# Kernel optimization log

Hardware: AMD Instinct MI355X
Metric: run time of the kernel (lower is better)

## Reference

```python
import jax, jax.numpy as jnp
import numpy as np

D_IN = 256
D_OUT = 256

def setup_inputs() -> dict:
    key = jax.random.key(0)
    kx, kq, kk, kv = jax.random.split(key, 4)
    x = jax.random.normal(kx, (8, D_IN, 64, 64), dtype=jnp.float32)
    s = 1.0 / np.sqrt(D_IN)
    Wq = jax.random.normal(kq, (D_OUT, D_IN), dtype=jnp.float32) * s
    Wk = jax.random.normal(kk, (D_OUT, D_IN), dtype=jnp.float32) * s
    Wv = jax.random.normal(kv, (D_OUT, D_IN), dtype=jnp.float32) * s
    return {"x": x, "Wq": Wq, "Wk": Wk, "Wv": Wv}

def reference(x, Wq, Wk, Wv):
    b, c_in, h, w = x.shape
    c = Wq.shape[0]
    # 1x1 conv == channel linear; tokens along N = h*w
    xt = x.reshape(b, c_in, h * w).transpose(0, 2, 1)      # (b, N, c_in)
    q = jnp.einsum('bnc,dc->bnd', xt, Wq)                  # (b, N, c)
    k = jnp.einsum('bnc,dc->bnd', xt, Wk)
    v = jnp.einsum('bnc,dc->bnd', xt, Wv)
    wei = jnp.einsum('bnd,bmd->bnm', q, k) / jnp.sqrt(jnp.asarray(c, x.dtype))
    wei = jax.nn.softmax(wei, axis=-1)
    out = jnp.einsum('bnm,bmd->bnd', wei, v)               # (b, N, c)
    return out.transpose(0, 2, 1).reshape(b, c, h, w)
```

## Files before the change

kernel.cpp:

```cpp
#include <hip/hip_runtime.h>

#define DIN 256
#define NTOK 4096

typedef __bf16 bf16;
typedef __bf16 bf16x8 __attribute__((ext_vector_type(8)));
typedef float floatx16 __attribute__((ext_vector_type(16)));

__device__ inline floatx16 mfma32(bf16x8 a, bf16x8 b, floatx16 c) {
    return __builtin_amdgcn_mfma_f32_32x32x16_bf16(a, b, c, 0, 0, 0);
}

__device__ inline void async16(const void* g, void* l) {
    __builtin_amdgcn_global_load_lds(
        (const __attribute__((address_space(1))) unsigned int*)g,
        (__attribute__((address_space(3))) unsigned int*)l, 16, 0, 0);
}

__global__ void convert_w(const float* __restrict__ wq, const float* __restrict__ wk,
                          const float* __restrict__ wv, bf16* __restrict__ Wb) {
    int i = blockIdx.x * 256 + threadIdx.x;
    const float* src = (i < 65536) ? wq : (i < 131072 ? wk : wv);
    Wb[i] = (bf16)src[i & 65535];
}

__global__ __launch_bounds__(256, 2) void proj_kernel(
    const float* __restrict__ x, const bf16* __restrict__ Wb,
    bf16* __restrict__ Qo, bf16* __restrict__ Ko, bf16* __restrict__ Vo)
{
    __shared__ bf16 xs[64][264];
    __shared__ bf16 wsm[64][264];

    int bid = blockIdx.x;
    int b = bid & 7, nt = bid >> 3;
    int n0 = nt * 64;
    int t = threadIdx.x;
    int lane = t & 63, w = t >> 6;
    int l32 = lane & 31, h = lane >> 5;
    int tokg = w >> 1;
    int og   = w & 1;

    {
        const float* xb = x + (size_t)b * DIN * NTOK;
#pragma unroll
        for (int it = 0; it < 16; ++it) {
            int flat = it * 256 + t;
            int c = flat >> 4;
            int nf = flat & 15;
            float4 v = *(const float4*)(xb + (size_t)c * NTOK + n0 + nf * 4);
            int nn = nf * 4;
            xs[nn + 0][c] = (bf16)v.x;
            xs[nn + 1][c] = (bf16)v.y;
            xs[nn + 2][c] = (bf16)v.z;
            xs[nn + 3][c] = (bf16)v.w;
        }
    }
    __syncthreads();

    bf16x8 xf[16];
#pragma unroll
    for (int ks = 0; ks < 16; ++ks)
        xf[ks] = *(const bf16x8*)&xs[tokg * 32 + l32][ks * 16 + h * 8];

    for (int mat = 0; mat < 3; ++mat) {
        const bf16* Wm = Wb + mat * 65536;
        for (int dg = 0; dg < 4; ++dg) {
            __syncthreads();
#pragma unroll
            for (int it = 0; it < 8; ++it) {
                int flat = it * 256 + t;
                int r = flat >> 5;
                int cs = (flat & 31) * 8;
                *(bf16x8*)&wsm[r][cs] =
                    *(const bf16x8*)(Wm + (size_t)(dg * 64 + r) * 256 + cs);
            }
            __syncthreads();

            floatx16 acc;
#pragma unroll
            for (int i = 0; i < 16; ++i) acc[i] = 0.0f;

            if (mat < 2) {
#pragma unroll
                for (int ks = 0; ks < 16; ++ks) {
                    bf16x8 wf = *(const bf16x8*)&wsm[og * 32 + l32][ks * 16 + h * 8];
                    acc = mfma32(xf[ks], wf, acc);
                }
                bf16* Out = (mat == 0 ? Qo : Ko) + (size_t)b * NTOK * DIN;
                int d = dg * 64 + og * 32 + l32;
#pragma unroll
                for (int r = 0; r < 16; ++r) {
                    int tok = n0 + tokg * 32 + (r & 3) + 8 * (r >> 2) + 4 * h;
                    Out[(size_t)tok * DIN + d] = (bf16)acc[r];
                }
            } else {
#pragma unroll
                for (int ks = 0; ks < 16; ++ks) {
                    bf16x8 wf = *(const bf16x8*)&wsm[og * 32 + l32][ks * 16 + h * 8];
                    acc = mfma32(wf, xf[ks], acc);
                }
                bf16* Out = Vo + (size_t)b * DIN * NTOK;
                int tok = n0 + tokg * 32 + l32;
#pragma unroll
                for (int r = 0; r < 16; ++r) {
                    int d = dg * 64 + og * 32 + (r & 3) + 8 * (r >> 2) + 4 * h;
                    Out[(size_t)d * NTOK + tok] = (bf16)acc[r];
                }
            }
        }
    }
}

__global__ __launch_bounds__(512, 2) void attn_kernel(
    const bf16* __restrict__ Q, const bf16* __restrict__ K,
    const bf16* __restrict__ V, float* __restrict__ out)
{
    __shared__ bf16 Ks[2][64][256];
    __shared__ bf16 Vs[2][256][64];
    __shared__ bf16 Ps[128][64];

    int bid = blockIdx.x;
    int b = bid & 7, qt = bid >> 3;
    int n0 = qt * 128;
    int t = threadIdx.x, lane = t & 63, w = t >> 6;
    int l32 = lane & 31, h = lane >> 5;

    const bf16* Qb = Q + (size_t)b * NTOK * DIN;
    const bf16* Kb = K + (size_t)b * NTOK * DIN;
    const bf16* Vb = V + (size_t)b * DIN * NTOK;
    float* Lp = (float*)&Ks[0][0][0];

    if (w < 4) {
        int tokg = w >> 1, mg = w & 1;
        int krow = mg * 32 + l32, kxr = l32 & 7;

        int koff[8];
#pragma unroll
        for (int jj = 0; jj < 8; ++jj) {
            int q = w * 8 + jj;
            int r = q * 2 + (lane >> 5);
            int ck = (lane & 31) ^ (r & 7);
            koff[jj] = (r * 256 + ck * 8) * 2;
        }

        bf16x8 qf[2][16];
#pragma unroll
        for (int ca = 0; ca < 2; ++ca) {
            const bf16* qrow = Qb + (size_t)(n0 + tokg * 64 + ca * 32 + l32) * DIN + h * 8;
#pragma unroll
            for (int ks = 0; ks < 16; ++ks) qf[ca][ks] = *(const bf16x8*)(qrow + ks * 16);
        }

        float lsum[2][16];
#pragma unroll
        for (int ca = 0; ca < 2; ++ca)
            for (int r = 0; r < 16; ++r) lsum[ca][r] = 0.0f;

#pragma unroll
        for (int jj = 0; jj < 8; ++jj) {
            async16((const char*)Kb + koff[jj], (bf16*)Ks[0] + (w * 8 + jj) * 512);
            async16((const char*)Kb + 32768 + koff[jj], (bf16*)Ks[1] + (w * 8 + jj) * 512);
        }
        __syncthreads();

        bf16x8 pe[2][2];
        {
            const bf16* Krd = (const bf16*)Ks[0] + krow * 256;
            floatx16 sa, sb;
#pragma unroll
            for (int i = 0; i < 16; ++i) { sa[i] = 0.0f; sb[i] = 0.0f; }
#pragma unroll
            for (int ks = 0; ks < 16; ++ks) {
                bf16x8 kf = *(const bf16x8*)(Krd + (((2 * ks + h) ^ kxr) * 8));
                sa = mfma32(qf[0][ks], kf, sa);
                sb = mfma32(qf[1][ks], kf, sb);
            }
#pragma unroll
            for (int ca = 0; ca < 2; ++ca)
#pragma unroll
                for (int r = 0; r < 16; ++r) {
                    float sv = (ca ? sb[r] : sa[r]);
                    bf16 e = (bf16)__expf(sv * 0.0625f);
                    pe[ca][r >> 3][r & 7] = e;
                    lsum[ca][r] += (float)e;
                }
#pragma unroll
            for (int ca = 0; ca < 2; ++ca)
#pragma unroll
                for (int r = 0; r < 16; ++r) {
                    int tok = tokg * 64 + ca * 32 + (r & 3) + 8 * (r >> 2) + 4 * h;
                    int key = (r & 3) + 4 * h;
                    Ps[tok][((mg * 4 + (l32 >> 3)) ^ key) * 8 + (l32 & 7)] = pe[ca][r >> 3][r & 7];
                }
        }
        __syncthreads();

#pragma unroll 2
        for (int mt = 0; mt < 64; ++mt) {
            if (mt < 62) {
                int kadd = ((mt + 2) & 63) * 32768;
#pragma unroll
                for (int jj = 0; jj < 8; ++jj)
                    async16((const char*)Kb + kadd + koff[jj],
                            (bf16*)Ks[mt & 1] + (w * 8 + jj) * 512);
            }
            const bf16* Krd = (const bf16*)Ks[(mt + 1) & 1] + krow * 256;
            floatx16 sa, sb;
#pragma unroll
            for (int i = 0; i < 16; ++i) { sa[i] = 0.0f; sb[i] = 0.0f; }
#pragma unroll
            for (int ks = 0; ks < 16; ++ks) {
                bf16x8 kf = *(const bf16x8*)(Krd + (((2 * ks + h) ^ kxr) * 8));
                sa = mfma32(qf[0][ks], kf, sa);
                sb = mfma32(qf[1][ks], kf, sb);
            }
#pragma unroll
            for (int ca = 0; ca < 2; ++ca)
#pragma unroll
                for (int r = 0; r < 16; ++r) {
                    float sv = (ca ? sb[r] : sa[r]);
                    bf16 e = (bf16)__expf(sv * 0.0625f);
                    pe[ca][r >> 3][r & 7] = e;
                    if (mt < 63) lsum[ca][r] += (float)e;
                }
            __syncthreads();
#pragma unroll
            for (int ca = 0; ca < 2; ++ca)
#pragma unroll
                for (int r = 0; r < 16; ++r) {
                    int tok = tokg * 64 + ca * 32 + (r & 3) + 8 * (r >> 2) + 4 * h;
                    int key = (r & 3) + 4 * h;
                    Ps[tok][((mg * 4 + (l32 >> 3)) ^ key) * 8 + (l32 & 7)] = pe[ca][r >> 3][r & 7];
                }
            __syncthreads();
        }

#pragma unroll
        for (int ca = 0; ca < 2; ++ca)
#pragma unroll
            for (int r = 0; r < 16; ++r) {
                float sv = lsum[ca][r];
                sv += __shfl_xor(sv, 1);
                sv += __shfl_xor(sv, 2);
                sv += __shfl_xor(sv, 4);
                sv += __shfl_xor(sv, 8);
                sv += __shfl_xor(sv, 16);
                lsum[ca][r] = sv;
            }
        if (l32 == 0) {
#pragma unroll
            for (int ca = 0; ca < 2; ++ca)
#pragma unroll
                for (int r = 0; r < 16; ++r)
                    Lp[mg * 128 + tokg * 64 + ca * 32 + (r & 3) + 8 * (r >> 2) + 4 * h] = lsum[ca][r];
        }
        __syncthreads();
    } else {
        int slab = w - 4;
        int dxr = l32 & 7, pxr = l32 & 7;

        int vofs[8];
#pragma unroll
        for (int jj = 0; jj < 8; ++jj) {
            int q = slab * 8 + jj;
            int d = q * 8 + (lane >> 3);
            int cv = (lane & 7) ^ (d & 7);
            vofs[jj] = (d * 4096 + cv * 8) * 2;
        }

        floatx16 oacc[8];
#pragma unroll
        for (int i = 0; i < 8; ++i)
            for (int j = 0; j < 16; ++j) oacc[i][j] = 0.0f;

#pragma unroll
        for (int jj = 0; jj < 8; ++jj)
            async16((const char*)Vb + vofs[jj], (bf16*)Vs[0] + (slab * 8 + jj) * 512);
        __syncthreads();
        __syncthreads();

#pragma unroll 2
        for (int mt = 0; mt < 64; ++mt) {
            if (mt < 63) {
                int vadd = (mt + 1) * 128;
#pragma unroll
                for (int jj = 0; jj < 8; ++jj)
                    async16((const char*)Vb + vadd + vofs[jj],
                            (bf16*)Vs[(mt + 1) & 1] + (slab * 8 + jj) * 512);
            }
            const bf16* Vrd = (const bf16*)Vs[mt & 1];
#pragma unroll
            for (int kst = 0; kst < 4; ++kst) {
                int ch = kst * 2 + h;
                bf16x8 pb[4], va[2];
#pragma unroll
                for (int tc = 0; tc < 4; ++tc)
                    pb[tc] = *(const bf16x8*)&Ps[tc * 32 + l32][((ch ^ pxr) * 8)];
#pragma unroll
                for (int dc = 0; dc < 2; ++dc)
                    va[dc] = *(const bf16x8*)(Vrd + (slab * 64 + dc * 32 + l32) * 64 + ((ch ^ dxr) * 8));
#pragma unroll
                for (int dc = 0; dc < 2; ++dc)
#pragma unroll
                    for (int tc = 0; tc < 4; ++tc)
                        oacc[dc * 4 + tc] = mfma32(va[dc], pb[tc], oacc[dc * 4 + tc]);
            }
            __syncthreads();
            __syncthreads();
        }

        __syncthreads();
        float* ob = out + (size_t)b * DIN * NTOK;
#pragma unroll
        for (int tc = 0; tc < 4; ++tc) {
            int tok = tc * 32 + l32;
            float rinv = 1.0f / (Lp[tok] + Lp[128 + tok]);
#pragma unroll
            for (int dc = 0; dc < 2; ++dc)
#pragma unroll
                for (int r = 0; r < 16; ++r) {
                    int d = slab * 64 + dc * 32 + (r & 3) + 8 * (r >> 2) + 4 * h;
                    ob[(size_t)d * NTOK + n0 + tok] = oacc[dc * 4 + tc][r] * rinv;
                }
        }
    }
}

extern "C" void kernel_launch(void* const* d_in, const int* in_sizes, int n_in,
                              void* d_out, int out_size, void* d_ws, size_t ws_size,
                              hipStream_t stream) {
    const float* x  = (const float*)d_in[0];
    const float* wq = (const float*)d_in[1];
    const float* wk = (const float*)d_in[2];
    const float* wv = (const float*)d_in[3];
    float* outf = (float*)d_out;

    char* ws = (char*)d_ws;
    bf16* Wb = (bf16*)(ws);
    bf16* Qp = (bf16*)(ws + (1u << 20));
    bf16* Kp = (bf16*)(ws + (1u << 20) + (16u << 20));
    bf16* Vp = (bf16*)(ws + (1u << 20) + (32u << 20));

    convert_w<<<768, 256, 0, stream>>>(wq, wk, wv, Wb);
    proj_kernel<<<512, 256, 0, stream>>>(x, Wb, Qp, Kp, Vp);
    attn_kernel<<<256, 512, 0, stream>>>(Qp, Kp, Vp, outf);
}
```

Before: 263.9 us.

## Double-buffer P tile and drop one barrier per key tile in attention loop

Makes the probability tile P double-buffered so producer waves write the next P while consumer waves read the current one, which cuts the per-iteration barriers from two to one. It also swaps the QK^T MFMA operand order so each lane holds contiguous key columns for one token, which allows packed bf16x4 stores to P and collapses the row-sum reduction to a single cross-half shuffle. The LDS XOR swizzle gains an extra row-dependent term for K, V and P to reduce bank conflicts. LDS use grows by another P buffer, which could affect occupancy at two blocks per CU, and the row-sum storage moves from the K buffer into the P buffer.

```diff
diff --git a/kernel.cpp b/kernel.cpp
--- a/kernel.cpp
+++ b/kernel.cpp
@@ -4,6 +4,7 @@
 #define NTOK 4096
 
 typedef __bf16 bf16;
+typedef __bf16 bf16x4 __attribute__((ext_vector_type(4)));
 typedef __bf16 bf16x8 __attribute__((ext_vector_type(8)));
 typedef float floatx16 __attribute__((ext_vector_type(16)));
 
@@ -117,29 +118,30 @@
 {
     __shared__ bf16 Ks[2][64][256];
     __shared__ bf16 Vs[2][256][64];
-    __shared__ bf16 Ps[128][64];
+    __shared__ bf16 Ps[2][128][64];
 
     int bid = blockIdx.x;
     int b = bid & 7, qt = bid >> 3;
     int n0 = qt * 128;
     int t = threadIdx.x, lane = t & 63, w = t >> 6;
     int l32 = lane & 31, h = lane >> 5;
+    int lkey = (l32 & 7) ^ ((l32 >> 3) & 3);
 
     const bf16* Qb = Q + (size_t)b * NTOK * DIN;
     const bf16* Kb = K + (size_t)b * NTOK * DIN;
     const bf16* Vb = V + (size_t)b * DIN * NTOK;
-    float* Lp = (float*)&Ks[0][0][0];
+    float* Lp = (float*)&Ps[0][0][0];
 
     if (w < 4) {
         int tokg = w >> 1, mg = w & 1;
-        int krow = mg * 32 + l32, kxr = l32 & 7;
+        int krow = mg * 32 + l32;
 
         int koff[8];
 #pragma unroll
         for (int jj = 0; jj < 8; ++jj) {
             int q = w * 8 + jj;
             int r = q * 2 + (lane >> 5);
-            int ck = (lane & 31) ^ (r & 7);
+            int ck = (lane & 31) ^ ((r & 7) ^ ((r >> 3) & 3));
             koff[jj] = (r * 256 + ck * 8) * 2;
         }
 
@@ -151,10 +153,7 @@
             for (int ks = 0; ks < 16; ++ks) qf[ca][ks] = *(const bf16x8*)(qrow + ks * 16);
         }
 
-        float lsum[2][16];
-#pragma unroll
-        for (int ca = 0; ca < 2; ++ca)
-            for (int r = 0; r < 16; ++r) lsum[ca][r] = 0.0f;
+        float lsum[2] = {0.0f, 0.0f};
 
 #pragma unroll
         for (int jj = 0; jj < 8; ++jj) {
@@ -163,108 +162,94 @@
         }
         __syncthreads();
 
-        bf16x8 pe[2][2];
         {
             const bf16* Krd = (const bf16*)Ks[0] + krow * 256;
-            floatx16 sa, sb;
-#pragma unroll
-            for (int i = 0; i < 16; ++i) { sa[i] = 0.0f; sb[i] = 0.0f; }
+            floatx16 st[2];
+#pragma unroll
+            for (int i = 0; i < 16; ++i) { st[0][i] = 0.0f; st[1][i] = 0.0f; }
 #pragma unroll
             for (int ks = 0; ks < 16; ++ks) {
-                bf16x8 kf = *(const bf16x8*)(Krd + (((2 * ks + h) ^ kxr) * 8));
-                sa = mfma32(qf[0][ks], kf, sa);
-                sb = mfma32(qf[1][ks], kf, sb);
-            }
-#pragma unroll
-            for (int ca = 0; ca < 2; ++ca)
-#pragma unroll
-                for (int r = 0; r < 16; ++r) {
-                    float sv = (ca ? sb[r] : sa[r]);
-                    bf16 e = (bf16)__expf(sv * 0.0625f);
-                    pe[ca][r >> 3][r & 7] = e;
-                    lsum[ca][r] += (float)e;
-                }
-#pragma unroll
-            for (int ca = 0; ca < 2; ++ca)
-#pragma unroll
-                for (int r = 0; r < 16; ++r) {
-                    int tok = tokg * 64 + ca * 32 + (r & 3) + 8 * (r >> 2) + 4 * h;
-                    int key = (r & 3) + 4 * h;
-                    Ps[tok][((mg * 4 + (l32 >> 3)) ^ key) * 8 + (l32 & 7)] = pe[ca][r >> 3][r & 7];
-                }
-        }
-        __syncthreads();
-
-#pragma unroll 2
+                bf16x8 kf = *(const bf16x8*)(Krd + (((2 * ks + h) ^ lkey) * 8));
+                st[0] = mfma32(kf, qf[0][ks], st[0]);
+                st[1] = mfma32(kf, qf[1][ks], st[1]);
+            }
+#pragma unroll
+            for (int ca = 0; ca < 2; ++ca) {
+                bf16* Prow = (bf16*)Ps[0] + (tokg * 64 + ca * 32 + l32) * 64;
+                float tsum = 0.0f;
+#pragma unroll
+                for (int g = 0; g < 4; ++g) {
+                    bf16x4 pk;
+#pragma unroll
+                    for (int i = 0; i < 4; ++i) {
+                        float e = __expf(st[ca][g * 4 + i] * 0.0625f);
+                        tsum += e;
+                        pk[i] = (bf16)e;
+                    }
+                    *(bf16x4*)((char*)Prow + (((mg * 4 + g) ^ lkey) * 16) + h * 8) = pk;
+                }
+                lsum[ca] += tsum;
+            }
+        }
+        __syncthreads();
+
         for (int mt = 0; mt < 64; ++mt) {
             if (mt < 62) {
-                int kadd = ((mt + 2) & 63) * 32768;
+                int kadd = (mt + 2) * 32768;
 #pragma unroll
                 for (int jj = 0; jj < 8; ++jj)
                     async16((const char*)Kb + kadd + koff[jj],
                             (bf16*)Ks[mt & 1] + (w * 8 + jj) * 512);
             }
-            const bf16* Krd = (const bf16*)Ks[(mt + 1) & 1] + krow * 256;
-            floatx16 sa, sb;
-#pragma unroll
-            for (int i = 0; i < 16; ++i) { sa[i] = 0.0f; sb[i] = 0.0f; }
-#pragma unroll
-            for (int ks = 0; ks < 16; ++ks) {
-                bf16x8 kf = *(const bf16x8*)(Krd + (((2 * ks + h) ^ kxr) * 8));
-                sa = mfma32(qf[0][ks], kf, sa);
-                sb = mfma32(qf[1][ks], kf, sb);
-            }
-#pragma unroll
-            for (int ca = 0; ca < 2; ++ca)
-#pragma unroll
-                for (int r = 0; r < 16; ++r) {
-                    float sv = (ca ? sb[r] : sa[r]);
-                    bf16 e = (bf16)__expf(sv * 0.0625f);
-                    pe[ca][r >> 3][r & 7] = e;
-                    if (mt < 63) lsum[ca][r] += (float)e;
-                }
+            if (mt < 63) {
+                const bf16* Krd = (const bf16*)Ks[(mt + 1) & 1] + krow * 256;
+                floatx16 st[2];
+#pragma unroll
+                for (int i = 0; i < 16; ++i) { st[0][i] = 0.0f; st[1][i] = 0.0f; }
+#pragma unroll
+                for (int ks = 0; ks < 16; ++ks) {
+                    bf16x8 kf = *(const bf16x8*)(Krd + (((2 * ks + h) ^ lkey) * 8));
+                    st[0] = mfma32(kf, qf[0][ks], st[0]);
+                    st[1] = mfma32(kf, qf[1][ks], st[1]);
+                }
+                bf16* Pw = (bf16*)Ps[(mt + 1) & 1];
+#pragma unroll
+                for (int ca = 0; ca < 2; ++ca) {
+                    bf16* Prow = Pw + (tokg * 64 + ca * 32 + l32) * 64;
+                    float tsum = 0.0f;
+#pragma unroll
+                    for (int g = 0; g < 4; ++g) {
+                        bf16x4 pk;
+#pragma unroll
+                        for (int i = 0; i < 4; ++i) {
+                            float e = __expf(st[ca][g * 4 + i] * 0.0625f);
+                            tsum += e;
+                            pk[i] = (bf16)e;
+                        }
+                        *(bf16x4*)((char*)Prow + (((mg * 4 + g) ^ lkey) * 16) + h * 8) = pk;
+                    }
+                    lsum[ca] += tsum;
+                }
+            }
             __syncthreads();
-#pragma unroll
-            for (int ca = 0; ca < 2; ++ca)
-#pragma unroll
-                for (int r = 0; r < 16; ++r) {
-                    int tok = tokg * 64 + ca * 32 + (r & 3) + 8 * (r >> 2) + 4 * h;
-                    int key = (r & 3) + 4 * h;
-                    Ps[tok][((mg * 4 + (l32 >> 3)) ^ key) * 8 + (l32 & 7)] = pe[ca][r >> 3][r & 7];
-                }
-            __syncthreads();
-        }
-
-#pragma unroll
-        for (int ca = 0; ca < 2; ++ca)
-#pragma unroll
-            for (int r = 0; r < 16; ++r) {
-                float sv = lsum[ca][r];
-                sv += __shfl_xor(sv, 1);
-                sv += __shfl_xor(sv, 2);
-                sv += __shfl_xor(sv, 4);
-                sv += __shfl_xor(sv, 8);
-                sv += __shfl_xor(sv, 16);
-                lsum[ca][r] = sv;
-            }
-        if (l32 == 0) {
-#pragma unroll
-            for (int ca = 0; ca < 2; ++ca)
-#pragma unroll
-                for (int r = 0; r < 16; ++r)
-                    Lp[mg * 128 + tokg * 64 + ca * 32 + (r & 3) + 8 * (r >> 2) + 4 * h] = lsum[ca][r];
+        }
+
+#pragma unroll
+        for (int ca = 0; ca < 2; ++ca) {
+            float sv = lsum[ca];
+            sv += __shfl_xor(sv, 32);
+            if (h == 0) Lp[mg * 128 + tokg * 64 + ca * 32 + l32] = sv;
         }
         __syncthreads();
     } else {
         int slab = w - 4;
-        int dxr = l32 & 7, pxr = l32 & 7;
 
         int vofs[8];
 #pragma unroll
         for (int jj = 0; jj < 8; ++jj) {
             int q = slab * 8 + jj;
             int d = q * 8 + (lane >> 3);
-            int cv = (lane & 7) ^ (d & 7);
+            int cv = (lane & 7) ^ ((d & 7) ^ ((d >> 3) & 3));
             vofs[jj] = (d * 4096 + cv * 8) * 2;
         }
 
@@ -279,7 +264,6 @@
         __syncthreads();
         __syncthreads();
 
-#pragma unroll 2
         for (int mt = 0; mt < 64; ++mt) {
             if (mt < 63) {
                 int vadd = (mt + 1) * 128;
@@ -289,23 +273,25 @@
                             (bf16*)Vs[(mt + 1) & 1] + (slab * 8 + jj) * 512);
             }
             const bf16* Vrd = (const bf16*)Vs[mt & 1];
+            const char* Prd = (const char*)Ps[mt & 1];
 #pragma unroll
             for (int kst = 0; kst < 4; ++kst) {
-                int ch = kst * 2 + h;
-                bf16x8 pb[4], va[2];
+                bf16x8 va[2], pb[4];
+#pragma unroll
+                for (int dc = 0; dc < 2; ++dc) {
+                    int d = slab * 64 + dc * 32 + l32;
+                    va[dc] = *(const bf16x8*)(Vrd + d * 64 + (((kst * 2 + h) ^ lkey) * 8));
+                }
 #pragma unroll
                 for (int tc = 0; tc < 4; ++tc)
-                    pb[tc] = *(const bf16x8*)&Ps[tc * 32 + l32][((ch ^ pxr) * 8)];
-#pragma unroll
-                for (int dc = 0; dc < 2; ++dc)
-                    va[dc] = *(const bf16x8*)(Vrd + (slab * 64 + dc * 32 + l32) * 64 + ((ch ^ dxr) * 8));
+                    pb[tc] = *(const bf16x8*)(Prd + (tc * 32 + l32) * 128 +
+                                              (((kst * 2 + h) ^ lkey) * 16));
 #pragma unroll
                 for (int dc = 0; dc < 2; ++dc)
 #pragma unroll
                     for (int tc = 0; tc < 4; ++tc)
                         oacc[dc * 4 + tc] = mfma32(va[dc], pb[tc], oacc[dc * 4 + tc]);
             }
-            __syncthreads();
             __syncthreads();
         }
 
```

Result: faster. 237.9 us (-9.8%).
